# Kernel tuning notes

Measured on AMD Instinct MI355X. Metric: run time of the kernel, lower is better.

Reference implementation:

```python
import jax, jax.numpy as jnp
import numpy as np
from jax import lax

N_NODES = 19
N_FILT = 8
CONV_CH = N_NODES * N_FILT  # 152
T = 512
POOL = 4
T_POOL = T // POOL  # 128
GCN_OUT = 16
FLAT = N_NODES * GCN_OUT * T_POOL  # 38912
HID = 128
N_CLS = 2
BN_EPS = 1e-5


def setup_inputs() -> dict:
    key = jax.random.key(0)
    ks = jax.random.split(key, 12)
    B = 1024
    x = jax.random.normal(ks[0], (B, N_NODES, T), dtype=jnp.float32)
    # grouped Conv1d(19 -> 152, k=5, groups=19): kernel (out_ch, in_ch/groups=1, k)
    conv_w = jax.random.normal(ks[1], (CONV_CH, 1, 5), dtype=jnp.float32) * 0.2
    conv_b = jax.random.normal(ks[2], (CONV_CH,), dtype=jnp.float32) * 0.05
    bn_gamma = jnp.ones((CONV_CH,), jnp.float32)
    bn_beta = jnp.zeros((CONV_CH,), jnp.float32)
    bn_mean = jax.random.normal(ks[3], (CONV_CH,), dtype=jnp.float32) * 0.1
    bn_var = jax.random.uniform(ks[4], (CONV_CH,), dtype=jnp.float32, minval=0.5, maxval=1.5)
    adj = jax.random.uniform(ks[5], (N_NODES, N_NODES), dtype=jnp.float32)
    gcn_w = jax.random.normal(ks[6], (GCN_OUT, N_FILT), dtype=jnp.float32) * (1.0 / np.sqrt(N_FILT))
    gcn_b = jnp.zeros((GCN_OUT,), jnp.float32)
    w1 = jax.random.normal(ks[7], (HID, FLAT), dtype=jnp.float32) * (1.0 / np.sqrt(FLAT))
    b1 = jnp.zeros((HID,), jnp.float32)
    w2 = jax.random.normal(ks[8], (N_CLS, HID), dtype=jnp.float32) * (1.0 / np.sqrt(HID))
    b2 = jnp.zeros((N_CLS,), jnp.float32)
    return dict(x=x, conv_w=conv_w, conv_b=conv_b, bn_gamma=bn_gamma, bn_beta=bn_beta,
                bn_mean=bn_mean, bn_var=bn_var, adj=adj, gcn_w=gcn_w, gcn_b=gcn_b,
                w1=w1, b1=b1, w2=w2, b2=b2)


def reference(x, conv_w, conv_b, bn_gamma, bn_beta, bn_mean, bn_var, adj,
              gcn_w, gcn_b, w1, b1, w2, b2):
    B = x.shape[0]
    # depthwise temporal conv: [B,19,T] -> [B,152,T]
    h = lax.conv_general_dilated(x, conv_w, window_strides=(1,), padding=[(2, 2)],
                                 feature_group_count=N_NODES,
                                 dimension_numbers=('NCW', 'OIW', 'NCW'))
    h = h + conv_b[None, :, None]
    # BatchNorm1d (eval mode: running stats) + ReLU, fused elementwise
    inv = bn_gamma / jnp.sqrt(bn_var + BN_EPS)
    h = jax.nn.relu(h * inv[None, :, None] + (bn_beta - bn_mean * inv)[None, :, None])
    # MaxPool1d(4): [B,152,512] -> [B,152,128]
    h = h.reshape(B, CONV_CH, T_POOL, POOL).max(axis=-1)
    # view -> [B,19,8,128]
    h = h.reshape(B, N_NODES, N_FILT, T_POOL)
    # softmax adjacency aggregation: bift = A_ij * bjft
    A = jax.nn.softmax(adj, axis=1)
    support = jnp.einsum('ij,bjft->bift', A, h)
    # permute to [B,19,128,8], linear 8->16, ReLU
    g = jax.nn.relu(jnp.einsum('bnft,of->bnto', support, gcn_w) + gcn_b)
    # classifier: flatten -> Linear(38912,128) -> ReLU -> (Dropout eval=identity) -> Linear(128,2)
    flat = g.reshape(B, FLAT)
    hid = jax.nn.relu(flat @ w1.T + b1)
    return hid @ w2.T + b2
```

## Files before the change

### kernel.cpp

```cpp
#include <hip/hip_runtime.h>

#define NB    1024
#define NN    19
#define NF    8
#define CCH   152
#define TLEN  512
#define TP    128
#define GO    16
#define KFLAT 38912
#define HID   128
#define NCLS  2
#define NROWS (NB*TP)
#define KC    152
#define KP    160
#define NJP   20
#define NOUT  304
#define GW    320
#define KW    (TP*GW)

#define KTILE 1024
#define NKT   (KW / KTILE)

typedef float  f32x4  __attribute__((ext_vector_type(4)));
typedef __bf16 bf16x8 __attribute__((ext_vector_type(8)));
typedef __bf16 bf16x4 __attribute__((ext_vector_type(4)));
typedef unsigned short u16x8 __attribute__((ext_vector_type(8)));

__global__ __launch_bounds__(256) void prep_small(
    const float* __restrict__ adj,
    const float* __restrict__ bn_gamma, const float* __restrict__ bn_beta,
    const float* __restrict__ bn_mean,  const float* __restrict__ bn_var,
    const float* __restrict__ conv_b,
    float* __restrict__ A_g, float* __restrict__ bnS, float* __restrict__ bnB)
{
    const int tid = threadIdx.x;
    if (tid < NN) {
        float v[NN];
        float m = -1e30f;
        #pragma unroll
        for (int j = 0; j < NN; ++j) { v[j] = adj[tid * NN + j]; m = fmaxf(m, v[j]); }
        float s = 0.f;
        #pragma unroll
        for (int j = 0; j < NN; ++j) { v[j] = expf(v[j] - m); s += v[j]; }
        float rc = 1.f / s;
        #pragma unroll
        for (int j = 0; j < NN; ++j) A_g[tid * NN + j] = v[j] * rc;
    }
    if (tid >= 64 && tid < 64 + CCH) {
        int c = tid - 64;
        float inv = bn_gamma[c] * rsqrtf(bn_var[c] + 1e-5f);
        bnS[c] = inv;
        bnB[c] = conv_b[c] * inv + bn_beta[c] - bn_mean[c] * inv;
    }
}

__global__ __launch_bounds__(256) void prep_m2(
    const float* __restrict__ A_g, const float* __restrict__ gcn_w,
    __bf16* __restrict__ m2g)
{
    int i = blockIdx.x * 256 + threadIdx.x;
    if (i >= GW * KP) return;
    int c = i / KP, k = i - c * KP;
    float v = 0.f;
    if (c < NOUT && k < KC) {
        int n = c >> 4, o = c & 15;
        int j = k >> 3, f = k & 7;
        v = A_g[n * NN + j] * gcn_w[o * NF + f];
    }
    m2g[i] = (__bf16)v;
}

__global__ __launch_bounds__(128) void conv_pool(
    const float* __restrict__ x,
    const float* __restrict__ conv_w,
    const float* __restrict__ bnS, const float* __restrict__ bnB,
    __bf16* __restrict__ H)
{
    const int bid = blockIdx.x;
    const int b = bid / NN, n = bid - b * NN;
    const int tp = threadIdx.x;

    const float* xr = x + ((size_t)b * NN + n) * TLEN;
    const float4 f4z = {0.f, 0.f, 0.f, 0.f};
    float4 L0 = (tp > 0)   ? *(const float4*)(xr + 4 * tp - 4) : f4z;
    float4 L1 =              *(const float4*)(xr + 4 * tp);
    float4 L2 = (tp < 127) ? *(const float4*)(xr + 4 * tp + 4) : f4z;
    float xv[9] = {L0.z, L0.w, L1.x, L1.y, L1.z, L1.w, L2.x, L2.y, L2.z};

    const float* cw = conv_w + n * (NF * 5);
    const float* Sp = bnS + n * NF;
    const float* Bp = bnB + n * NF;

    union { __bf16 h[8]; u16x8 v; } hv;
    #pragma unroll
    for (int f = 0; f < NF; ++f) {
        float w0 = cw[f*5+0], w1 = cw[f*5+1], w2 = cw[f*5+2], w3 = cw[f*5+3], w4 = cw[f*5+4];
        float s = Sp[f], bb = Bp[f];
        float m = -1e30f;
        #pragma unroll
        for (int p = 0; p < 4; ++p) {
            float a = xv[p]*w0 + xv[p+1]*w1 + xv[p+2]*w2 + xv[p+3]*w3 + xv[p+4]*w4;
            m = fmaxf(m, a * s + bb);
        }
        hv.h[f] = (__bf16)fmaxf(m, 0.f);
    }
    size_t row = (size_t)b * TP + tp;
    *(u16x8*)(H + ((size_t)n * NROWS + row) * 8) = hv.v;
    if (n == NN - 1) {
        u16x8 z = {0,0,0,0,0,0,0,0};
        *(u16x8*)(H + ((size_t)(NJP - 1) * NROWS + row) * 8) = z;
    }
}

__global__ __launch_bounds__(256) void mix_gcn(
    const __bf16* __restrict__ H,
    const __bf16* __restrict__ m2g,
    const float* __restrict__ gcn_b,
    __bf16* __restrict__ g2)
{
    const int tid  = threadIdx.x;
    const int lane = tid & 63, w = tid >> 6;
    const int arow = lane & 15;
    const int jg   = lane >> 4;
    const int ct0  = w * 5;

    const float4 gbv = *(const float4*)(gcn_b + jg * 4);

    bf16x8 mf[5][5];
    #pragma unroll
    for (int ct = 0; ct < 5; ++ct)
        #pragma unroll
        for (int ks = 0; ks < 5; ++ks)
            mf[ct][ks] = *(const bf16x8*)(
                m2g + (size_t)((ct0 + ct) * 16 + arow) * KP + ks * 32 + jg * 8);

    const int Rbase = blockIdx.x * 128;
    for (int it = 0; it < 8; ++it) {
        const int R0 = Rbase + it * 16;

        const __bf16* hp = H + (size_t)(R0 + arow) * 8;
        bf16x8 af[5];
        #pragma unroll
        for (int ks = 0; ks < 5; ++ks)
            af[ks] = *(const bf16x8*)(hp + (size_t)(ks * 4 + jg) * NROWS * 8);

        f32x4 acc[5];
        #pragma unroll
        for (int ct = 0; ct < 5; ++ct) acc[ct] = (f32x4){0.f, 0.f, 0.f, 0.f};

        #pragma unroll
        for (int ks = 0; ks < 5; ++ks)
            #pragma unroll
            for (int ct = 0; ct < 5; ++ct)
                acc[ct] = __builtin_amdgcn_mfma_f32_16x16x32_bf16(mf[ct][ks], af[ks], acc[ct], 0, 0, 0);

        __bf16* gp = g2 + (size_t)(R0 + arow) * GW + ct0 * 16 + jg * 4;
        #pragma unroll
        for (int ct = 0; ct < 5; ++ct) {
            bf16x4 v;
            v[0] = (__bf16)fmaxf(acc[ct][0] + gbv.x, 0.f);
            v[1] = (__bf16)fmaxf(acc[ct][1] + gbv.y, 0.f);
            v[2] = (__bf16)fmaxf(acc[ct][2] + gbv.z, 0.f);
            v[3] = (__bf16)fmaxf(acc[ct][3] + gbv.w, 0.f);
            *(bf16x4*)(gp + ct * 16) = v;
        }
    }
}

__global__ __launch_bounds__(256) void w1_permute(
    const float* __restrict__ w1, __bf16* __restrict__ w1p)
{
    int i = blockIdx.x * 256 + threadIdx.x;
    if (i >= HID * (KW / 8)) return;
    int j = i / 5120, rem = i - j * 5120;
    int t = rem / 40, c8 = rem - t * 40;
    bf16x8 r;
    if (c8 < 38) {
        int n = c8 >> 1, o0 = (c8 & 1) * 8;
        const float* src = w1 + (size_t)j * KFLAT + n * 2048 + t * 16 + o0;
        #pragma unroll
        for (int e = 0; e < 8; ++e) r[e] = (__bf16)src[e];
    } else {
        #pragma unroll
        for (int e = 0; e < 8; ++e) r[e] = (__bf16)0.f;
    }
    *(bf16x8*)(w1p + (size_t)i * 8) = r;
}

__global__ __launch_bounds__(256) void gemm_fc1(
    const __bf16* __restrict__ gmat,
    const __bf16* __restrict__ wmat,
    float* __restrict__ partial)
{
    __shared__ __align__(16) __bf16 At[128][40];
    __shared__ __align__(16) __bf16 Bt[128][40];

    const int tid = threadIdx.x;
    const int b0 = blockIdx.x * 128;
    const int k0 = blockIdx.y * KTILE;

    const int lane = tid & 63;
    const int w = tid >> 6;
    const int wm = (w >> 1) * 64;
    const int wn = (w & 1) * 64;

    const int srow = tid >> 2;
    const int soct = tid & 3;

    f32x4 acc[4][4];
    #pragma unroll
    for (int m = 0; m < 4; ++m)
        #pragma unroll
        for (int n = 0; n < 4; ++n) acc[m][n] = (f32x4){0.f, 0.f, 0.f, 0.f};

    const int arow = lane & 15;
    const int aoct = (lane >> 4) * 8;

    for (int ks = 0; ks < KTILE / 32; ++ks) {
        const int gk = k0 + ks * 32 + soct * 8;
        *(u16x8*)&At[srow     ][soct * 8] = *(const u16x8*)(gmat + (size_t)(b0 + srow     ) * KW + gk);
        *(u16x8*)&At[srow + 64][soct * 8] = *(const u16x8*)(gmat + (size_t)(b0 + srow + 64) * KW + gk);
        *(u16x8*)&Bt[srow     ][soct * 8] = *(const u16x8*)(wmat + (size_t)(srow     ) * KW + gk);
        *(u16x8*)&Bt[srow + 64][soct * 8] = *(const u16x8*)(wmat + (size_t)(srow + 64) * KW + gk);
        __syncthreads();

        bf16x8 af[4], bfr[4];
        #pragma unroll
        for (int m = 0; m < 4; ++m) af[m]  = *(const bf16x8*)&At[wm + m * 16 + arow][aoct];
        #pragma unroll
        for (int n = 0; n < 4; ++n) bfr[n] = *(const bf16x8*)&Bt[wn + n * 16 + arow][aoct];
        #pragma unroll
        for (int m = 0; m < 4; ++m)
            #pragma unroll
            for (int n = 0; n < 4; ++n)
                acc[m][n] = __builtin_amdgcn_mfma_f32_16x16x32_bf16(af[m], bfr[n], acc[m][n], 0, 0, 0);
        __syncthreads();
    }

    float* pout = partial + (size_t)blockIdx.y * (NB * HID);
    #pragma unroll
    for (int m = 0; m < 4; ++m) {
        const int rbase = b0 + wm + m * 16 + (lane >> 4) * 4;
        #pragma unroll
        for (int n = 0; n < 4; ++n) {
            const int col = wn + n * 16 + (lane & 15);
            #pragma unroll
            for (int r = 0; r < 4; ++r)
                pout[(size_t)(rbase + r) * HID + col] = acc[m][n][r];
        }
    }
}

__global__ __launch_bounds__(128) void reduce_fc2(
    const float* __restrict__ partial,
    const float* __restrict__ b1,
    const float* __restrict__ w2,
    const float* __restrict__ b2,
    float* __restrict__ out)
{
    __shared__ float red0[128], red1[128];
    const int b = blockIdx.x, j = threadIdx.x;
    float s = b1[j];
    #pragma unroll 4
    for (int p = 0; p < NKT; ++p) s += partial[(size_t)p * (NB * HID) + b * HID + j];
    float h = fmaxf(s, 0.f);
    red0[j] = h * w2[j];
    red1[j] = h * w2[HID + j];
    __syncthreads();
    for (int off = 64; off > 0; off >>= 1) {
        if (j < off) { red0[j] += red0[j + off]; red1[j] += red1[j + off]; }
        __syncthreads();
    }
    if (j == 0) {
        out[b * 2 + 0] = red0[0] + b2[0];
        out[b * 2 + 1] = red1[0] + b2[1];
    }
}

extern "C" void kernel_launch(void* const* d_in, const int* in_sizes, int n_in,
                              void* d_out, int out_size, void* d_ws, size_t ws_size,
                              hipStream_t stream) {
    const float* x        = (const float*)d_in[0];
    const float* conv_w   = (const float*)d_in[1];
    const float* conv_b   = (const float*)d_in[2];
    const float* bn_gamma = (const float*)d_in[3];
    const float* bn_beta  = (const float*)d_in[4];
    const float* bn_mean  = (const float*)d_in[5];
    const float* bn_var   = (const float*)d_in[6];
    const float* adj      = (const float*)d_in[7];
    const float* gcn_w    = (const float*)d_in[8];
    const float* gcn_b    = (const float*)d_in[9];
    const float* w1       = (const float*)d_in[10];
    const float* b1       = (const float*)d_in[11];
    const float* w2       = (const float*)d_in[12];
    const float* b2       = (const float*)d_in[13];
    float* out = (float*)d_out;

    char* ws = (char*)d_ws;
    __bf16* g2   = (__bf16*)ws;
    __bf16* Hbuf = (__bf16*)(ws + 83886080);
    __bf16* w1p  = (__bf16*)(ws + 83886080);
    float*  part = (float*)(ws + 94371840);
    __bf16* m2g  = (__bf16*)(ws + 125829120);
    float*  A_g  = (float*)(ws + 125931520);
    float*  bnS  = (float*)(ws + 125933568);
    float*  bnB  = (float*)(ws + 125934592);

    prep_small<<<dim3(1), dim3(256), 0, stream>>>(
        adj, bn_gamma, bn_beta, bn_mean, bn_var, conv_b, A_g, bnS, bnB);
    prep_m2<<<dim3(200), dim3(256), 0, stream>>>(A_g, gcn_w, m2g);
    conv_pool<<<dim3(NB * NN), dim3(128), 0, stream>>>(x, conv_w, bnS, bnB, Hbuf);
    mix_gcn<<<dim3(NROWS / 128), dim3(256), 0, stream>>>(Hbuf, m2g, gcn_b, g2);
    w1_permute<<<dim3(HID * (KW / 8) / 256), dim3(256), 0, stream>>>(w1, w1p);
    gemm_fc1<<<dim3(8, NKT), dim3(256), 0, stream>>>(g2, w1p, part);
    reduce_fc2<<<dim3(NB), dim3(128), 0, stream>>>(part, b1, w2, b2, out);
}
```

Before: 107.6 us.

## Store GCN output in natural flatten order and drop padded w1 permutation

The mix_gcn kernel now writes its output directly in the reference flatten layout (node, time, channel) with a KFLAT stride instead of a padded 320-wide per-time-row layout. As a result w1 only needs a straight fp32-to-bf16 conversion rather than a permuted, zero-padded copy. The fc1 GEMM's K dimension shrinks from 40960 to 38912, cutting GEMM work and intermediate traffic by the padding fraction. In exchange, the g2 stores become more scattered (16-channel chunks at node strides), and NKT changes, so reduce_fc2 now sums 38 partial tiles.

```diff
diff --git a/kernel.cpp b/kernel.cpp
--- a/kernel.cpp
+++ b/kernel.cpp
@@ -15,11 +15,10 @@
 #define KP    160
 #define NJP   20
 #define NOUT  304
-#define GW    320
-#define KW    (TP*GW)
+#define M2R   320
 
 #define KTILE 1024
-#define NKT   (KW / KTILE)
+#define NKT   (KFLAT / KTILE)
 
 typedef float  f32x4  __attribute__((ext_vector_type(4)));
 typedef __bf16 bf16x8 __attribute__((ext_vector_type(8)));
@@ -59,7 +58,7 @@
     __bf16* __restrict__ m2g)
 {
     int i = blockIdx.x * 256 + threadIdx.x;
-    if (i >= GW * KP) return;
+    if (i >= M2R * KP) return;
     int c = i / KP, k = i - c * KP;
     float v = 0.f;
     if (c < NOUT && k < KC) {
@@ -134,9 +133,10 @@
             mf[ct][ks] = *(const bf16x8*)(
                 m2g + (size_t)((ct0 + ct) * 16 + arow) * KP + ks * 32 + jg * 8);
 
-    const int Rbase = blockIdx.x * 128;
+    const int b = blockIdx.x;
     for (int it = 0; it < 8; ++it) {
-        const int R0 = Rbase + it * 16;
+        const int R0 = b * TP + it * 16;
+        const int t  = it * 16 + arow;
 
         const __bf16* hp = H + (size_t)(R0 + arow) * 8;
         bf16x8 af[5];
@@ -154,37 +154,32 @@
             for (int ct = 0; ct < 5; ++ct)
                 acc[ct] = __builtin_amdgcn_mfma_f32_16x16x32_bf16(mf[ct][ks], af[ks], acc[ct], 0, 0, 0);
 
-        __bf16* gp = g2 + (size_t)(R0 + arow) * GW + ct0 * 16 + jg * 4;
+        __bf16* gb2 = g2 + (size_t)b * KFLAT + t * 16 + jg * 4;
         #pragma unroll
         for (int ct = 0; ct < 5; ++ct) {
-            bf16x4 v;
-            v[0] = (__bf16)fmaxf(acc[ct][0] + gbv.x, 0.f);
-            v[1] = (__bf16)fmaxf(acc[ct][1] + gbv.y, 0.f);
-            v[2] = (__bf16)fmaxf(acc[ct][2] + gbv.z, 0.f);
-            v[3] = (__bf16)fmaxf(acc[ct][3] + gbv.w, 0.f);
-            *(bf16x4*)(gp + ct * 16) = v;
+            const int n = ct0 + ct;
+            if (n < NN) {
+                bf16x4 v;
+                v[0] = (__bf16)fmaxf(acc[ct][0] + gbv.x, 0.f);
+                v[1] = (__bf16)fmaxf(acc[ct][1] + gbv.y, 0.f);
+                v[2] = (__bf16)fmaxf(acc[ct][2] + gbv.z, 0.f);
+                v[3] = (__bf16)fmaxf(acc[ct][3] + gbv.w, 0.f);
+                *(bf16x4*)(gb2 + n * (TP * GO)) = v;
+            }
         }
     }
 }
 
-__global__ __launch_bounds__(256) void w1_permute(
-    const float* __restrict__ w1, __bf16* __restrict__ w1p)
-{
-    int i = blockIdx.x * 256 + threadIdx.x;
-    if (i >= HID * (KW / 8)) return;
-    int j = i / 5120, rem = i - j * 5120;
-    int t = rem / 40, c8 = rem - t * 40;
-    bf16x8 r;
-    if (c8 < 38) {
-        int n = c8 >> 1, o0 = (c8 & 1) * 8;
-        const float* src = w1 + (size_t)j * KFLAT + n * 2048 + t * 16 + o0;
-        #pragma unroll
-        for (int e = 0; e < 8; ++e) r[e] = (__bf16)src[e];
-    } else {
-        #pragma unroll
-        for (int e = 0; e < 8; ++e) r[e] = (__bf16)0.f;
-    }
-    *(bf16x8*)(w1p + (size_t)i * 8) = r;
+__global__ __launch_bounds__(256) void w1_to_bf16(
+    const float* __restrict__ w1, __bf16* __restrict__ o)
+{
+    const int n4 = (HID * KFLAT) >> 2;
+    for (int i = blockIdx.x * 256 + threadIdx.x; i < n4; i += gridDim.x * 256) {
+        float4 v = ((const float4*)w1)[i];
+        bf16x4 r;
+        r[0] = (__bf16)v.x; r[1] = (__bf16)v.y; r[2] = (__bf16)v.z; r[3] = (__bf16)v.w;
+        ((bf16x4*)o)[i] = r;
+    }
 }
 
 __global__ __launch_bounds__(256) void gemm_fc1(
@@ -218,10 +213,10 @@
 
     for (int ks = 0; ks < KTILE / 32; ++ks) {
         const int gk = k0 + ks * 32 + soct * 8;
-        *(u16x8*)&At[srow     ][soct * 8] = *(const u16x8*)(gmat + (size_t)(b0 + srow     ) * KW + gk);
-        *(u16x8*)&At[srow + 64][soct * 8] = *(const u16x8*)(gmat + (size_t)(b0 + srow + 64) * KW + gk);
-        *(u16x8*)&Bt[srow     ][soct * 8] = *(const u16x8*)(wmat + (size_t)(srow     ) * KW + gk);
-        *(u16x8*)&Bt[srow + 64][soct * 8] = *(const u16x8*)(wmat + (size_t)(srow + 64) * KW + gk);
+        *(u16x8*)&At[srow     ][soct * 8] = *(const u16x8*)(gmat + (size_t)(b0 + srow     ) * KFLAT + gk);
+        *(u16x8*)&At[srow + 64][soct * 8] = *(const u16x8*)(gmat + (size_t)(b0 + srow + 64) * KFLAT + gk);
+        *(u16x8*)&Bt[srow     ][soct * 8] = *(const u16x8*)(wmat + (size_t)(srow     ) * KFLAT + gk);
+        *(u16x8*)&Bt[srow + 64][soct * 8] = *(const u16x8*)(wmat + (size_t)(srow + 64) * KFLAT + gk);
         __syncthreads();
 
         bf16x8 af[4], bfr[4];
@@ -261,7 +256,7 @@
     __shared__ float red0[128], red1[128];
     const int b = blockIdx.x, j = threadIdx.x;
     float s = b1[j];
-    #pragma unroll 4
+    #pragma unroll 2
     for (int p = 0; p < NKT; ++p) s += partial[(size_t)p * (NB * HID) + b * HID + j];
     float h = fmaxf(s, 0.f);
     red0[j] = h * w2[j];
@@ -298,20 +293,20 @@
 
     char* ws = (char*)d_ws;
     __bf16* g2   = (__bf16*)ws;
-    __bf16* Hbuf = (__bf16*)(ws + 83886080);
-    __bf16* w1p  = (__bf16*)(ws + 83886080);
-    float*  part = (float*)(ws + 94371840);
-    __bf16* m2g  = (__bf16*)(ws + 125829120);
-    float*  A_g  = (float*)(ws + 125931520);
-    float*  bnS  = (float*)(ws + 125933568);
-    float*  bnB  = (float*)(ws + 125934592);
+    __bf16* Hbuf = (__bf16*)(ws + 79691776);
+    __bf16* w1b  = (__bf16*)(ws + 79691776);
+    float*  part = (float*)(ws + 89653248);
+    __bf16* m2g  = (__bf16*)(ws + 121634816);
+    float*  A_g  = (float*)(ws + 121737216);
+    float*  bnS  = (float*)(ws + 121739264);
+    float*  bnB  = (float*)(ws + 121740288);
 
     prep_small<<<dim3(1), dim3(256), 0, stream>>>(
         adj, bn_gamma, bn_beta, bn_mean, bn_var, conv_b, A_g, bnS, bnB);
     prep_m2<<<dim3(200), dim3(256), 0, stream>>>(A_g, gcn_w, m2g);
     conv_pool<<<dim3(NB * NN), dim3(128), 0, stream>>>(x, conv_w, bnS, bnB, Hbuf);
-    mix_gcn<<<dim3(NROWS / 128), dim3(256), 0, stream>>>(Hbuf, m2g, gcn_b, g2);
-    w1_permute<<<dim3(HID * (KW / 8) / 256), dim3(256), 0, stream>>>(w1, w1p);
-    gemm_fc1<<<dim3(8, NKT), dim3(256), 0, stream>>>(g2, w1p, part);
+    mix_gcn<<<dim3(NB), dim3(256), 0, stream>>>(Hbuf, m2g, gcn_b, g2);
+    w1_to_bf16<<<dim3(1024), dim3(256), 0, stream>>>(w1, w1b);
+    gemm_fc1<<<dim3(8, NKT), dim3(256), 0, stream>>>(g2, w1b, part);
     reduce_fc2<<<dim3(NB), dim3(128), 0, stream>>>(part, b1, w2, b2, out);
 }
```

New measurement: 111.3 us. 1.03x slower.
